# Performance work log

Hardware: AMD Instinct MI355X
Metric: run time of the kernel (lower is better)

Reference implementation:

```python
import jax, jax.numpy as jnp
import numpy as np

OUTPUT_SIZE = 16384          # number of map units (must be a perfect square)
SIDE = 128.0                 # sqrt(OUTPUT_SIZE)
SIGMA = 2.0                  # neighbourhood std-dev (non-trainable weight in original)
B, D = 2048, 256


def setup_inputs() -> dict:
    key = jax.random.key(0)
    k1, k2 = jax.random.split(key)
    x = jax.random.normal(k1, (B, D), dtype=jnp.float32)
    kernel = jax.random.normal(k2, (D, OUTPUT_SIZE), dtype=jnp.float32) * 0.1
    return {"x": x, "kernel": kernel}


def _grid_coords():
    # 2D coordinates of each flattened map unit: unit k -> (k // side, k % side)
    idx = jnp.arange(OUTPUT_SIZE, dtype=jnp.float32)
    return jnp.floor(idx / SIDE), jnp.mod(idx, SIDE)  # each (size,)


def reference(x, kernel):
    # Squared Euclidean distance of every sample to every prototype: (B, size).
    # Same math as tf.norm(x[:, :, None] - kernel[None])**2, expressed as a GEMM.
    norms2 = (jnp.sum(x * x, axis=1, keepdims=True)
              - 2.0 * (x @ kernel)
              + jnp.sum(kernel * kernel, axis=0, keepdims=True))
    norms2 = jnp.maximum(norms2, 0.0)

    # Winner-take-all unit per sample, mapped to 2D grid coordinates.
    wta = jnp.argmin(norms2, axis=1).astype(jnp.float32)        # (B,)
    mean_r = jnp.floor(wta / SIDE)                               # (B,)
    mean_c = jnp.mod(wta, SIDE)                                  # (B,)

    # Gaussian neighbourhood over the 2D grid, flattened: (B, size).
    gr, gc = _grid_coords()
    dr = gr[None, :] - mean_r[:, None]
    dc = gc[None, :] - mean_c[:, None]
    radials = jnp.exp(-0.5 / (SIGMA * SIGMA) * (dr * dr + dc * dc))

    return radials * norms2
```

## Files before the change

### kernel.cpp

```cpp
#include <hip/hip_runtime.h>
#include <hip/hip_fp16.h>

#define OUTN 16384
#define BATCH 2048
#define DIM   256

typedef _Float16 half8 __attribute__((ext_vector_type(8)));
typedef _Float16 half4 __attribute__((ext_vector_type(4)));
typedef float    floatx4 __attribute__((ext_vector_type(4)));
typedef unsigned long long u64;

__device__ __forceinline__ void gl2lds16(const void* g, void* l) {
    __builtin_amdgcn_global_load_lds(
        (const __attribute__((address_space(1))) void*)g,
        (__attribute__((address_space(3))) void*)l, 16, 0, 0);
}

__device__ __forceinline__ u64 packkey(float v, int col) {
    unsigned u = __float_as_uint(v);
    u = (u & 0x80000000u) ? ~u : (u | 0x80000000u);
    return ((u64)u << 32) | (unsigned)col;
}
__device__ __forceinline__ float unpackval(u64 p) {
    unsigned u = (unsigned)(p >> 32);
    u = (u & 0x80000000u) ? (u & 0x7fffffffu) : ~u;
    return __uint_as_float(u);
}

__global__ __launch_bounds__(256) void prep_all(
        const float* __restrict__ x, const float* __restrict__ kern,
        _Float16* __restrict__ xh, float* __restrict__ rown,
        _Float16* __restrict__ kT, float* __restrict__ colnp,
        float* __restrict__ kT32) {
    int blk = blockIdx.x, t = threadIdx.x;
    if (blk < 512) {
        __shared__ float tile[64][65];
        __shared__ float npart[4][64];
        int tx = t & 63, ty = t >> 6;
        int j0 = (blk >> 1) * 64;
        int dhalf = blk & 1, dbase = dhalf * 128;
        float nrm = 0.f;
        for (int pc = 0; pc < 2; pc++) {
            int dc = dbase + pc * 64;
            __syncthreads();
            for (int it = 0; it < 16; it++) {
                int d = dc + ty + it * 4;
                float v = kern[(size_t)d * OUTN + j0 + tx];
                tile[ty + it * 4][tx] = v;
                nrm = fmaf(v, v, nrm);
            }
            __syncthreads();
            for (int c = t; c < 512; c += 256) {
                int j = c >> 3, o8 = (c & 7) * 8;
                half8 h;
                for (int u = 0; u < 8; u++) h[u] = (_Float16)tile[o8 + u][j];
                *(half8*)&kT[(size_t)(j0 + j) * DIM + dc + o8] = h;
            }
            if (kT32) {
                for (int c = t; c < 1024; c += 256) {
                    int j = c >> 4, o4 = (c & 15) * 4;
                    floatx4 f = (floatx4){tile[o4][j], tile[o4 + 1][j],
                                          tile[o4 + 2][j], tile[o4 + 3][j]};
                    __builtin_nontemporal_store(f,
                        (floatx4*)&kT32[(size_t)(j0 + j) * DIM + dc + o4]);
                }
            }
        }
        npart[ty][tx] = nrm;
        __syncthreads();
        if (t < 64)
            colnp[(size_t)dhalf * OUTN + j0 + t] =
                npart[0][t] + npart[1][t] + npart[2][t] + npart[3][t];
    } else {
        int b = blk - 512;
        float v = x[b * DIM + t];
        xh[b * DIM + t] = (_Float16)v;
        float s = v * v;
        for (int off = 32; off; off >>= 1) s += __shfl_down(s, off, 64);
        __shared__ float wsum[4];
        if ((t & 63) == 0) wsum[t >> 6] = s;
        __syncthreads();
        if (t == 0) rown[b] = wsum[0] + wsum[1] + wsum[2] + wsum[3];
    }
}

template <bool NF16>
__global__ __launch_bounds__(256) void gemm_norms(
        const _Float16* __restrict__ xh, const _Float16* __restrict__ kT,
        const float* __restrict__ rown, const float* __restrict__ colnp,
        void* __restrict__ n2out, u64* __restrict__ blockcand) {
    __shared__ __align__(16) char smem[32768];
    _Float16* As = (_Float16*)smem;
    _Float16* Bs = (_Float16*)(smem + 16384);
    u64* cand = (u64*)smem;
    int tid  = threadIdx.x;
    int bid  = blockIdx.y * gridDim.x + blockIdx.x;
    int xcd  = bid & 7, kk = bid >> 3;
    int colblk = xcd * 16 + (kk & 15);
    int rowblk = kk >> 4;
    int col0 = colblk * 128;
    int row0 = rowblk * 128;
    int wid = tid >> 6, lane = tid & 63;
    int wr = wid >> 1, wc = wid & 1;
    int l15 = lane & 15, l4 = lane >> 4;
    int xh7 = l15 & 7;

    floatx4 acc[4][4];
    for (int i = 0; i < 4; i++)
        for (int j = 0; j < 4; j++)
            acc[i][j] = (floatx4){0.f, 0.f, 0.f, 0.f};

    for (int kt = 0; kt < 4; kt++) {
        int k0 = kt * 64;
        for (int it = 0; it < 4; it++) {
            int chunk = it * 256 + tid;
            int r = chunk >> 3, gg = chunk & 7;
            int ksw = (gg ^ (r & 7)) * 8;
            gl2lds16(&xh[(size_t)(row0 + r) * DIM + k0 + ksw], &As[chunk * 8]);
            gl2lds16(&kT[(size_t)(col0 + r) * DIM + k0 + ksw], &Bs[chunk * 8]);
        }
        __syncthreads();
        for (int s = 0; s < 2; s++) {
            int g = s * 4 + l4;
            int sw = (g ^ xh7) * 8;
            half8 af[4], bf[4];
            for (int i = 0; i < 4; i++)
                af[i] = *(half8*)&As[(wr * 64 + i * 16 + l15) * 64 + sw];
            for (int j = 0; j < 4; j++)
                bf[j] = *(half8*)&Bs[(wc * 64 + j * 16 + l15) * 64 + sw];
            for (int i = 0; i < 4; i++)
                for (int j = 0; j < 4; j++)
                    acc[i][j] = __builtin_amdgcn_mfma_f32_16x16x32_f16(
                        af[i], bf[j], acc[i][j], 0, 0, 0);
        }
        __syncthreads();
    }

    float cn[4]; int oc[4];
    int cid = wc * 16 + l15;
    for (int j = 0; j < 4; j++) {
        oc[j] = col0 + wc * 64 + j * 16 + l15;
        cn[j] = colnp[oc[j]] + colnp[OUTN + oc[j]];
    }
    for (int i = 0; i < 4; i++) {
        for (int r = 0; r < 4; r++) {
            int row_l = wr * 64 + i * 16 + l4 * 4 + r;
            int orow  = row0 + row_l;
            float rn = rown[orow];
            u64 best = ~0ull;
            for (int j = 0; j < 4; j++) {
                float val = rn + cn[j] - 2.0f * acc[i][j][r];
                size_t oi = (size_t)orow * OUTN + oc[j];
                if (NF16) __builtin_nontemporal_store((_Float16)val,
                              (_Float16*)n2out + oi);
                else      __builtin_nontemporal_store(val, (float*)n2out + oi);
                u64 p = packkey(val, oc[j]);
                if (p < best) best = p;
            }
            cand[row_l * 32 + (cid ^ (row_l & 31))] = best;
        }
    }
    __syncthreads();
    if (tid < 128) {
        u64 m1 = ~0ull, m2 = ~0ull;
        for (int s = 0; s < 32; s++) {
            u64 v = cand[tid * 32 + (s ^ (tid & 31))];
            if (v < m1) { m2 = m1; m1 = v; }
            else if (v < m2) { m2 = v; }
        }
        size_t base = (size_t)(row0 + tid) * 256 + colblk * 2;
        blockcand[base]     = m1;
        blockcand[base + 1] = m2;
    }
}

template <bool NF16, bool KT32P>
__global__ __launch_bounds__(256) void refine_finalize(
        const u64* __restrict__ blockcand, const float* __restrict__ x,
        const float* __restrict__ kern, const float* __restrict__ colnp,
        const float* __restrict__ kT32, const void* __restrict__ n2in,
        float* __restrict__ out) {
    int b = blockIdx.x, t = threadIdx.x;
    __shared__ float xrow[DIM];
    __shared__ u64 wred[4];
    xrow[t] = x[b * DIM + t];
    u64 e = blockcand[(size_t)b * 256 + t];

    u64 m = e;
    for (int off = 32; off; off >>= 1) {
        u64 o = __shfl_xor(m, off, 64);
        if (o < m) m = o;
    }
    if ((t & 63) == 0) wred[t >> 6] = m;
    __syncthreads();
    u64 g0 = wred[0] < wred[1] ? wred[0] : wred[1];
    u64 g1 = wred[2] < wred[3] ? wred[2] : wred[3];
    float minv = unpackval(g0 < g1 ? g0 : g1);

    float ve = unpackval(e);
    u64 p = ~0ull;
    if (ve <= minv + 0.125f) {
        int j = (int)(e & 0xffffffffu);
        if (KT32P) {
            float d0 = 0.f, d1 = 0.f, d2 = 0.f, d3 = 0.f;
            const floatx4* kc = (const floatx4*)&kT32[(size_t)j * DIM];
            for (int d4 = 0; d4 < DIM / 4; d4++) {
                floatx4 kv = kc[d4];
                d0 = fmaf(xrow[d4 * 4 + 0], kv[0], d0);
                d1 = fmaf(xrow[d4 * 4 + 1], kv[1], d1);
                d2 = fmaf(xrow[d4 * 4 + 2], kv[2], d2);
                d3 = fmaf(xrow[d4 * 4 + 3], kv[3], d3);
            }
            float dot = (d0 + d1) + (d2 + d3);
            p = packkey((colnp[j] + colnp[OUTN + j]) - 2.0f * dot, j);
        } else {
            float dot = 0.f;
            for (int d = 0; d < DIM; d++)
                dot = fmaf(xrow[d], kern[(size_t)d * OUTN + j], dot);
            p = packkey((colnp[j] + colnp[OUTN + j]) - 2.0f * dot, j);
        }
    }
    __syncthreads();
    u64 m2 = p;
    for (int off = 32; off; off >>= 1) {
        u64 o = __shfl_xor(m2, off, 64);
        if (o < m2) m2 = o;
    }
    if ((t & 63) == 0) wred[t >> 6] = m2;
    __syncthreads();
    u64 h0 = wred[0] < wred[1] ? wred[0] : wred[1];
    u64 h1 = wred[2] < wred[3] ? wred[2] : wred[3];
    int w = (int)((h0 < h1 ? h0 : h1) & 0xffffffffu);
    int wrr = w >> 7, wcc = w & 127;

    const _Float16* r16 = (const _Float16*)n2in + (size_t)b * OUTN;
    const float*    r32 = (const float*)n2in    + (size_t)b * OUTN;
    float* rowp = out + (size_t)b * OUTN;

    int c0 = (t & 31) * 4, rb = t >> 5;
    int dc0 = c0 - wcc;
    int q0 = dc0 * dc0, q1 = (dc0 + 1) * (dc0 + 1),
        q2 = (dc0 + 2) * (dc0 + 2), q3 = (dc0 + 3) * (dc0 + 3);
    int qmin = min(min(q0, q1), min(q2, q3));
    float ec0 = __expf(-0.125f * (float)q0), ec1 = __expf(-0.125f * (float)q1),
          ec2 = __expf(-0.125f * (float)q2), ec3 = __expf(-0.125f * (float)q3);

    for (int it = 0; it < 16; it++) {
        int idx4 = it * 256 + t;
        int r = it * 8 + rb;
        int dr = r - wrr, drsq = dr * dr;
        floatx4 res = (floatx4){0.f, 0.f, 0.f, 0.f};
        if (drsq + qmin <= 720) {
            float va, vb, vc, vd;
            if (NF16) {
                half4 h = *(const half4*)&r16[idx4 * 4];
                va = (float)h[0]; vb = (float)h[1]; vc = (float)h[2]; vd = (float)h[3];
            } else {
                floatx4 f = ((const floatx4*)r32)[idx4];
                va = f[0]; vb = f[1]; vc = f[2]; vd = f[3];
            }
            float er = __expf(-0.125f * (float)drsq);
            if (drsq + q0 <= 720) res[0] = er * ec0 * fmaxf(va, 0.f);
            if (drsq + q1 <= 720) res[1] = er * ec1 * fmaxf(vb, 0.f);
            if (drsq + q2 <= 720) res[2] = er * ec2 * fmaxf(vc, 0.f);
            if (drsq + q3 <= 720) res[3] = er * ec3 * fmaxf(vd, 0.f);
        }
        __builtin_nontemporal_store(res, (floatx4*)rowp + idx4);
    }
}

extern "C" void kernel_launch(void* const* d_in, const int* in_sizes, int n_in,
                              void* d_out, int out_size, void* d_ws, size_t ws_size,
                              hipStream_t stream) {
    const float* x    = (const float*)d_in[0];
    const float* kern = (const float*)d_in[1];
    float* out = (float*)d_out;
    char* ws = (char*)d_ws;

    _Float16* xh   = (_Float16*)(ws);
    _Float16* kT   = (_Float16*)(ws + (1u << 20));
    float*   colnp = (float*)(ws + (9u << 20));
    float*   rown  = (float*)(ws + (9u << 20) + (128u << 10));
    u64* blockcand = (u64*)(ws + (10u << 20));
    void*    n2h   = (void*)(ws + (14u << 20));
    bool f16path  = ws_size >= ((size_t)78 << 20);
    bool kt32path = ws_size >= ((size_t)94 << 20);
    float* kT32 = kt32path ? (float*)(ws + (78u << 20)) : nullptr;

    prep_all<<<2560, 256, 0, stream>>>(x, kern, xh, rown, kT, colnp, kT32);
    if (f16path) {
        gemm_norms<true><<<dim3(OUTN / 128, BATCH / 128), 256, 0, stream>>>(
            xh, kT, rown, colnp, n2h, blockcand);
        if (kt32path)
            refine_finalize<true, true><<<BATCH, 256, 0, stream>>>(
                blockcand, x, kern, colnp, kT32, n2h, out);
        else
            refine_finalize<true, false><<<BATCH, 256, 0, stream>>>(
                blockcand, x, kern, colnp, nullptr, n2h, out);
    } else {
        gemm_norms<false><<<dim3(OUTN / 128, BATCH / 128), 256, 0, stream>>>(
            xh, kT, rown, colnp, (void*)out, blockcand);
        refine_finalize<false, false><<<BATCH, 256, 0, stream>>>(
            blockcand, x, kern, colnp, nullptr, (const void*)out, out);
    }
}
```

Baseline: 228.0 us.

## Double-buffer GEMM LDS tiles with K=32 stages and use regular n2 stores

Rewrites the GEMM main loop to use two LDS buffers of K=32 slices, prefetching the next slice via global_load_lds while MFMAs run on the current one. The XOR swizzle is dropped and synchronisation drops from two barriers per 64-wide K step to one per 32-wide step. The intermediate norms stores switch from nontemporal to normal stores, so the later radial kernel may hit in cache. Risks include LDS bank conflicts from the unswizzled 64-byte rows, and the prefetch may race with reads of the other buffer since the barrier is only at the loop end.

```diff
diff --git a/kernel.cpp b/kernel.cpp
--- a/kernel.cpp
+++ b/kernel.cpp
@@ -90,8 +90,6 @@
         const float* __restrict__ rown, const float* __restrict__ colnp,
         void* __restrict__ n2out, u64* __restrict__ blockcand) {
     __shared__ __align__(16) char smem[32768];
-    _Float16* As = (_Float16*)smem;
-    _Float16* Bs = (_Float16*)(smem + 16384);
     u64* cand = (u64*)smem;
     int tid  = threadIdx.x;
     int bid  = blockIdx.y * gridDim.x + blockIdx.x;
@@ -103,38 +101,49 @@
     int wid = tid >> 6, lane = tid & 63;
     int wr = wid >> 1, wc = wid & 1;
     int l15 = lane & 15, l4 = lane >> 4;
-    int xh7 = l15 & 7;
+
+    int c0 = tid, c1 = tid + 256;
+    int rA0 = c0 >> 2, gA0 = c0 & 3;
+    int rA1 = c1 >> 2, gA1 = c1 & 3;
+    const _Float16* srcA0 = &xh[(size_t)(row0 + rA0) * DIM + gA0 * 8];
+    const _Float16* srcA1 = &xh[(size_t)(row0 + rA1) * DIM + gA1 * 8];
+    const _Float16* srcB0 = &kT[(size_t)(col0 + rA0) * DIM + gA0 * 8];
+    const _Float16* srcB1 = &kT[(size_t)(col0 + rA1) * DIM + gA1 * 8];
 
     floatx4 acc[4][4];
     for (int i = 0; i < 4; i++)
         for (int j = 0; j < 4; j++)
             acc[i][j] = (floatx4){0.f, 0.f, 0.f, 0.f};
 
-    for (int kt = 0; kt < 4; kt++) {
-        int k0 = kt * 64;
-        for (int it = 0; it < 4; it++) {
-            int chunk = it * 256 + tid;
-            int r = chunk >> 3, gg = chunk & 7;
-            int ksw = (gg ^ (r & 7)) * 8;
-            gl2lds16(&xh[(size_t)(row0 + r) * DIM + k0 + ksw], &As[chunk * 8]);
-            gl2lds16(&kT[(size_t)(col0 + r) * DIM + k0 + ksw], &Bs[chunk * 8]);
-        }
+#define STAGE(buf, kt) do {                                                    \
+        _Float16* A_ = (_Float16*)smem + (buf) * 8192;                         \
+        _Float16* B_ = A_ + 4096;                                              \
+        int ko_ = (kt) * 32;                                                   \
+        gl2lds16(srcA0 + ko_, A_ + c0 * 8);                                    \
+        gl2lds16(srcA1 + ko_, A_ + c1 * 8);                                    \
+        gl2lds16(srcB0 + ko_, B_ + c0 * 8);                                    \
+        gl2lds16(srcB1 + ko_, B_ + c1 * 8);                                    \
+    } while (0)
+
+    STAGE(0, 0);
+    __syncthreads();
+    for (int kt = 0; kt < 8; kt++) {
+        int cur = kt & 1;
+        if (kt < 7) STAGE(cur ^ 1, kt + 1);
+        const _Float16* A = (const _Float16*)smem + cur * 8192;
+        const _Float16* B = A + 4096;
+        half8 af[4], bf[4];
+        for (int i = 0; i < 4; i++)
+            af[i] = *(half8*)&A[(wr * 64 + i * 16 + l15) * 32 + l4 * 8];
+        for (int j = 0; j < 4; j++)
+            bf[j] = *(half8*)&B[(wc * 64 + j * 16 + l15) * 32 + l4 * 8];
+        for (int i = 0; i < 4; i++)
+            for (int j = 0; j < 4; j++)
+                acc[i][j] = __builtin_amdgcn_mfma_f32_16x16x32_f16(
+                    af[i], bf[j], acc[i][j], 0, 0, 0);
         __syncthreads();
-        for (int s = 0; s < 2; s++) {
-            int g = s * 4 + l4;
-            int sw = (g ^ xh7) * 8;
-            half8 af[4], bf[4];
-            for (int i = 0; i < 4; i++)
-                af[i] = *(half8*)&As[(wr * 64 + i * 16 + l15) * 64 + sw];
-            for (int j = 0; j < 4; j++)
-                bf[j] = *(half8*)&Bs[(wc * 64 + j * 16 + l15) * 64 + sw];
-            for (int i = 0; i < 4; i++)
-                for (int j = 0; j < 4; j++)
-                    acc[i][j] = __builtin_amdgcn_mfma_f32_16x16x32_f16(
-                        af[i], bf[j], acc[i][j], 0, 0, 0);
-        }
-        __syncthreads();
-    }
+    }
+#undef STAGE
 
     float cn[4]; int oc[4];
     int cid = wc * 16 + l15;
@@ -151,9 +160,8 @@
             for (int j = 0; j < 4; j++) {
                 float val = rn + cn[j] - 2.0f * acc[i][j][r];
                 size_t oi = (size_t)orow * OUTN + oc[j];
-                if (NF16) __builtin_nontemporal_store((_Float16)val,
-                              (_Float16*)n2out + oi);
-                else      __builtin_nontemporal_store(val, (float*)n2out + oi);
+                if (NF16) ((_Float16*)n2out)[oi] = (_Float16)val;
+                else      ((float*)n2out)[oi]    = val;
                 u64 p = packkey(val, oc[j]);
                 if (p < best) best = p;
             }
@@ -237,8 +245,8 @@
     const float*    r32 = (const float*)n2in    + (size_t)b * OUTN;
     float* rowp = out + (size_t)b * OUTN;
 
-    int c0 = (t & 31) * 4, rb = t >> 5;
-    int dc0 = c0 - wcc;
+    int cc0 = (t & 31) * 4, rb = t >> 5;
+    int dc0 = cc0 - wcc;
     int q0 = dc0 * dc0, q1 = (dc0 + 1) * (dc0 + 1),
         q2 = (dc0 + 2) * (dc0 + 2), q3 = (dc0 + 3) * (dc0 + 3);
     int qmin = min(min(q0, q1), min(q2, q3));
```

Result: faster. 210.6 us (-7.6%).
